# Kernel optimization log

Hardware: AMD Instinct MI355X
Metric: run time of the kernel (lower is better)

## Reference

```python
import jax, jax.numpy as jnp
import numpy as np

EPS = 1e-12  # torch F.normalize eps


def setup_inputs() -> dict:
    key = jax.random.key(0)
    k1, k2 = jax.random.split(key)
    B, C, H, W = 8, 512, 96, 144
    M, D = 512, 512
    query_source = jax.random.normal(k1, (B, C, H, W), dtype=jnp.float32)
    mem = jax.random.uniform(k2, (M, D), dtype=jnp.float32)
    # Memory params are initialized as F.normalize(rand, dim=1)
    mem = mem / jnp.maximum(jnp.linalg.norm(mem, axis=1, keepdims=True), EPS)
    return {"query_source": query_source, "memory": mem}


def reference(query_source, memory):
    # forward(query_source, keys, only_update=False, query_target=None, fusion_keys=None)
    # -> self.read(normalize(query_source).permute(0,2,3,1), memory['3_0'])
    # L2-normalize over channel dim (dim=1), like F.normalize
    norm = jnp.linalg.norm(query_source, axis=1, keepdims=True)
    q = query_source / jnp.maximum(norm, EPS)
    q = jnp.transpose(q, (0, 2, 3, 1))  # [B, H, W, D]
    B, H, W, D = q.shape
    M = memory.shape[0]
    # get_score: score = query @ mem^T, then softmax over tokens (dim 0) and slots (dim 1)
    score = jnp.einsum('nd,md->nm', q.reshape(B * H * W, D), memory)  # [N, M]
    softmax_score_query = jax.nn.softmax(score, axis=0)
    softmax_score_memory = jax.nn.softmax(score, axis=1)
    # read: updated_query = score_memory.detach() @ memory
    updated_query = jax.lax.stop_gradient(softmax_score_memory) @ memory  # [N, D]
    updated_query = updated_query.reshape(B, H, W, D).transpose(0, 3, 1, 2)  # [B, D, H, W]
    return updated_query, softmax_score_query, softmax_score_memory
```

## Files before the change

### kernel.cpp

```cpp
#include <hip/hip_runtime.h>
#include <hip/hip_bf16.h>
#include <cstdint>
#include <cstddef>

#define HWIMG 13824
#define NTOK  110592
#define CDIM  512

typedef float  floatx4  __attribute__((ext_vector_type(4)));
typedef __bf16 bf16x8   __attribute__((ext_vector_type(8)));
typedef unsigned short ushortx8 __attribute__((ext_vector_type(8)));

__device__ __forceinline__ unsigned short f2bf(float f) {
  unsigned int u = __float_as_uint(f);
  u += 0x7FFFu + ((u >> 16) & 1u);
  return (unsigned short)(u >> 16);
}
__device__ __forceinline__ float bf2f(unsigned short u) {
  return __uint_as_float(((unsigned int)u) << 16);
}

#define GLL16(g, l)                                                                \
  __builtin_amdgcn_global_load_lds((const __attribute__((address_space(1))) void*)(g), \
                                   (__attribute__((address_space(3))) void*)(l), 16, 0, 0)

__global__ __launch_bounds__(256) void convert_mem_kernel(
    const float* __restrict__ mem, unsigned short* __restrict__ membf,
    unsigned short* __restrict__ memTbf) {
  int g = blockIdx.x * 256 + threadIdx.x;
  int m = g >> 9, d = g & 511;
  unsigned short b = f2bf(mem[g]);
  membf[g] = b;
  memTbf[d * 512 + m] = b;
}

__global__ __launch_bounds__(256) void normalize_kernel(
    const float* __restrict__ qs, unsigned short* __restrict__ qbf) {
  __shared__ float red[4][64];
  __shared__ float inv[64];
  __shared__ float tile[64][65];
  const int t = threadIdx.x;
  const int n0 = blockIdx.x * 64;
  const int b = n0 / HWIMG;
  const int r0 = n0 % HWIMG;
  const float* base = qs + (size_t)b * 512 * HWIMG + r0;
  const int tok = t & 63, cp = t >> 6;

  float ssq = 0.f;
  for (int c = cp; c < 512; c += 4) {
    float x = base[(size_t)c * HWIMG + tok];
    ssq += x * x;
  }
  red[cp][tok] = ssq;
  __syncthreads();
  if (t < 64) {
    float s = red[0][t] + red[1][t] + red[2][t] + red[3][t];
    inv[t] = 1.0f / fmaxf(sqrtf(s), 1e-12f);
  }
  __syncthreads();

  for (int cc = 0; cc < 8; cc++) {
#pragma unroll
    for (int i = 0; i < 16; i++) {
      int cl = (t >> 6) + i * 4;
      tile[cl][tok] = base[(size_t)(cc * 64 + cl) * HWIMG + tok];
    }
    __syncthreads();
    const int c_out = t & 63;
    const int tg = t >> 6;
#pragma unroll
    for (int i = 0; i < 16; i++) {
      int tk = tg * 16 + i;
      float v = tile[c_out][tk] * inv[tk];
      qbf[(size_t)(n0 + tk) * 512 + cc * 64 + c_out] = f2bf(v);
    }
    __syncthreads();
  }
}

#define GEMM_STAGE8(gAp, gBp, kb)                                          \
  GLL16((gAp) + (kb), lA);                                                 \
  GLL16((gAp) + (kb) + 32768, lA + 4096);                                  \
  GLL16((gAp) + (kb) + 65536, lA + 8192);                                  \
  GLL16((gAp) + (kb) + 98304, lA + 12288);                                 \
  GLL16((gBp) + (kb), lB);                                                 \
  GLL16((gBp) + (kb) + 32768, lB + 4096);                                  \
  GLL16((gBp) + (kb) + 65536, lB + 8192);                                  \
  GLL16((gBp) + (kb) + 98304, lB + 12288);

#define GEMM_K_LOOP(gAp, gBp)                                              \
  for (int kb = 0; kb < 1024; kb += 128) {                                 \
    GEMM_STAGE8(gAp, gBp, kb)                                              \
    asm volatile("s_waitcnt vmcnt(0)" ::: "memory");                       \
    __syncthreads();                                                       \
    _Pragma("unroll")                                                      \
    for (int h = 0; h < 2; h++) {                                          \
      bf16x8 af[4], bfv[4];                                                \
      _Pragma("unroll")                                                    \
      for (int i = 0; i < 4; i++)                                          \
        af[i] = *(const bf16x8*)&Alds[((((am + i) * 2 + h) << 6) | lane) * 8]; \
      _Pragma("unroll")                                                    \
      for (int j = 0; j < 4; j++)                                          \
        bfv[j] = *(const bf16x8*)&Blds[((((bn + j) * 2 + h) << 6) | lane) * 8]; \
      _Pragma("unroll")                                                    \
      for (int i = 0; i < 4; i++)                                          \
        _Pragma("unroll")                                                  \
        for (int j = 0; j < 4; j++)                                        \
          acc[i][j] = __builtin_amdgcn_mfma_f32_16x16x32_bf16(             \
              af[i], bfv[j], acc[i][j], 0, 0, 0);                          \
    }                                                                      \
    __syncthreads();                                                       \
  }

#define GEMM_COMMON_DECLS                                                  \
  __shared__ unsigned short Alds[128 * 64];                                \
  __shared__ unsigned short Blds[128 * 64];                                \
  const int t = threadIdx.x;                                               \
  const int lane = t & 63, wid = t >> 6;                                   \
  const int quad = lane >> 4, li = lane & 15;                              \
  const int n0 = blockIdx.x * 128;                                         \
  const int am = (wid & 1) * 4, bn = (wid >> 1) * 4;                       \
  const int wm = (wid & 1) * 64, wn = (wid >> 1) * 64;                     \
  const int row0 = ((t >> 7) << 4) | (t & 15);                             \
  const int koff = ((t >> 6) & 1) * 64 + ((t >> 4) & 3) * 16;              \
  char* lA = (char*)Alds + t * 16;                                         \
  char* lB = (char*)Blds + t * 16;

__global__ __launch_bounds__(256) void gemm1_kernel(
    const unsigned short* __restrict__ A, const unsigned short* __restrict__ Bm,
    unsigned short* __restrict__ Ebf, float* __restrict__ colsum,
    float* __restrict__ rowsum) {
  __shared__ float cs_lds[512];
  __shared__ float rs_lds[128];
  GEMM_COMMON_DECLS
  cs_lds[t] = 0.f; cs_lds[t + 256] = 0.f;
  if (t < 128) rs_lds[t] = 0.f;
  const char* gA = (const char*)A + (size_t)(n0 + row0) * 1024 + koff;
  const char* gB0 = (const char*)Bm + (size_t)row0 * 1024 + koff;
  float racc[4][4];
#pragma unroll
  for (int i = 0; i < 4; i++)
#pragma unroll
    for (int r = 0; r < 4; r++) racc[i][r] = 0.f;

#pragma unroll 1
  for (int mt = 0; mt < 4; mt++) {
    floatx4 acc[4][4];
    {
      floatx4 z = {0.f, 0.f, 0.f, 0.f};
#pragma unroll
      for (int i = 0; i < 4; i++)
#pragma unroll
        for (int j = 0; j < 4; j++) acc[i][j] = z;
    }
    const char* gB = gB0 + (size_t)mt * 131072;
    GEMM_K_LOOP(gA, gB)

    float cp[4] = {0.f, 0.f, 0.f, 0.f};
#pragma unroll
    for (int i = 0; i < 4; i++) {
#pragma unroll
      for (int r = 0; r < 4; r++) {
        const int row = n0 + wm + i * 16 + quad * 4 + r;
        float rowacc = 0.f;
#pragma unroll
        for (int j = 0; j < 4; j++) {
          float e = __expf(acc[i][j][r]);
          const int col = mt * 128 + wn + j * 16 + li;
          Ebf[(size_t)row * 512 + col] = f2bf(e);
          cp[j] += e;
          rowacc += e;
        }
        racc[i][r] += rowacc;
      }
    }
#pragma unroll
    for (int j = 0; j < 4; j++) {
      float c = cp[j];
      c += __shfl_xor(c, 16, 64);
      c += __shfl_xor(c, 32, 64);
      if (lane < 16) atomicAdd(&cs_lds[mt * 128 + wn + j * 16 + li], c);
    }
  }

#pragma unroll
  for (int i = 0; i < 4; i++) {
#pragma unroll
    for (int r = 0; r < 4; r++) {
      float v = racc[i][r];
      v += __shfl_xor(v, 1, 64);
      v += __shfl_xor(v, 2, 64);
      v += __shfl_xor(v, 4, 64);
      v += __shfl_xor(v, 8, 64);
      if (li == 0) atomicAdd(&rs_lds[wm + i * 16 + quad * 4 + r], v);
    }
  }
  __syncthreads();
  if (t < 128) rowsum[n0 + t] = rs_lds[t];
  atomicAdd(&colsum[t], cs_lds[t]);
  atomicAdd(&colsum[t + 256], cs_lds[t + 256]);
}

__global__ __launch_bounds__(256) void gemm2_kernel(
    const unsigned short* __restrict__ P, const unsigned short* __restrict__ BmT,
    const float* __restrict__ rowsum, float* __restrict__ out0) {
  GEMM_COMMON_DECLS
  const char* gA = (const char*)P + (size_t)(n0 + row0) * 1024 + koff;
  const char* gB0 = (const char*)BmT + (size_t)row0 * 1024 + koff;
  floatx4 rinv[4];
#pragma unroll
  for (int i = 0; i < 4; i++) {
    floatx4 one = {1.f, 1.f, 1.f, 1.f};
    rinv[i] = one / *(const floatx4*)&rowsum[n0 + wm + i * 16 + quad * 4];
  }
  const int bimg = n0 / HWIMG;
  const int r0 = n0 % HWIMG;

#pragma unroll 1
  for (int mt = 0; mt < 4; mt++) {
    floatx4 acc[4][4];
    {
      floatx4 z = {0.f, 0.f, 0.f, 0.f};
#pragma unroll
      for (int i = 0; i < 4; i++)
#pragma unroll
        for (int j = 0; j < 4; j++) acc[i][j] = z;
    }
    const char* gB = gB0 + (size_t)mt * 131072;
    GEMM_K_LOOP(gA, gB)

#pragma unroll
    for (int i = 0; i < 4; i++) {
      const int rb = r0 + wm + i * 16 + quad * 4;
#pragma unroll
      for (int j = 0; j < 4; j++) {
        const int col = mt * 128 + wn + j * 16 + li;
        *(floatx4*)&out0[(size_t)(bimg * 512 + col) * HWIMG + rb] =
            acc[i][j] * rinv[i];
      }
    }
  }
}

__global__ __launch_bounds__(256) void finalize_kernel(
    const unsigned short* __restrict__ Ebf, const float* __restrict__ colsum,
    const float* __restrict__ rowsum, float* __restrict__ out1,
    float* __restrict__ out2) {
  const int t = threadIdx.x;
  const int lane = t & 63, wid = t >> 6;
  const int rowbase = (blockIdx.x * 4 + wid) * 16;
  const int c0 = lane * 8;
  floatx4 one = {1.f, 1.f, 1.f, 1.f};
  floatx4 rc0 = one / *(const floatx4*)&colsum[c0];
  floatx4 rc1 = one / *(const floatx4*)&colsum[c0 + 4];
#pragma unroll 4
  for (int it = 0; it < 16; it++) {
    const int row = rowbase + it;
    const size_t off = (size_t)row * 512 + c0;
    ushortx8 ev = *(const ushortx8*)&Ebf[off];
    floatx4 e0, e1;
    e0[0] = bf2f(ev[0]); e0[1] = bf2f(ev[1]); e0[2] = bf2f(ev[2]); e0[3] = bf2f(ev[3]);
    e1[0] = bf2f(ev[4]); e1[1] = bf2f(ev[5]); e1[2] = bf2f(ev[6]); e1[3] = bf2f(ev[7]);
    float rr = 1.0f / rowsum[row];
    *(floatx4*)&out1[off]     = e0 * rc0;
    *(floatx4*)&out1[off + 4] = e1 * rc1;
    *(floatx4*)&out2[off]     = e0 * rr;
    *(floatx4*)&out2[off + 4] = e1 * rr;
  }
}

extern "C" void kernel_launch(void* const* d_in, const int* in_sizes, int n_in,
                              void* d_out, int out_size, void* d_ws, size_t ws_size,
                              hipStream_t stream) {
  const float* qs  = (const float*)d_in[0];
  const float* mem = (const float*)d_in[1];

  float* out0 = (float*)d_out;
  float* out1 = out0 + (size_t)NTOK * 512;
  float* out2 = out1 + (size_t)NTOK * 512;

  char* ws = (char*)d_ws;
  unsigned short* qbf    = (unsigned short*)ws;
  unsigned short* Ebf    = (unsigned short*)(ws + 113246208);
  unsigned short* membf  = (unsigned short*)(ws + 226492416);
  unsigned short* memTbf = (unsigned short*)(ws + 227016704);
  float* colsum          = (float*)(ws + 227540992);
  float* rowsum          = (float*)(ws + 227543040);

  hipMemsetAsync(colsum, 0, 2048, stream);
  convert_mem_kernel<<<1024, 256, 0, stream>>>(mem, membf, memTbf);
  normalize_kernel<<<NTOK / 64, 256, 0, stream>>>(qs, qbf);
  gemm1_kernel<<<NTOK / 128, 256, 0, stream>>>(qbf, membf, Ebf, colsum, rowsum);
  finalize_kernel<<<NTOK / 64, 256, 0, stream>>>(Ebf, colsum, rowsum, out1, out2);
  gemm2_kernel<<<NTOK / 128, 256, 0, stream>>>(Ebf, memTbf, rowsum, out0);
}
```

Measured before the change: 1.229 ms.

## Double-buffer GEMM K-loop and fuse finalize into gemm2 via staged LDS tiles

Both GEMMs now stream their K and M tiles as one flat loop of 32 stages, using a two-buffer LDS pipeline so global-to-LDS loads of the next stage overlap the MFMA work on the current one. The separate finalize kernel is removed. gemm2 now builds both softmax outputs from the E tiles it already has in LDS during its first 8 stages, scaling by the inverse column and row sums. This avoids re-reading the bf16 E matrix from HBM and one kernel launch. In exchange LDS use doubles to 64KB per block, and gemm2 gets more output store traffic inside the GEMM loop.

```diff
diff --git a/kernel.cpp b/kernel.cpp
--- a/kernel.cpp
+++ b/kernel.cpp
@@ -78,43 +78,8 @@
   }
 }
 
-#define GEMM_STAGE8(gAp, gBp, kb)                                          \
-  GLL16((gAp) + (kb), lA);                                                 \
-  GLL16((gAp) + (kb) + 32768, lA + 4096);                                  \
-  GLL16((gAp) + (kb) + 65536, lA + 8192);                                  \
-  GLL16((gAp) + (kb) + 98304, lA + 12288);                                 \
-  GLL16((gBp) + (kb), lB);                                                 \
-  GLL16((gBp) + (kb) + 32768, lB + 4096);                                  \
-  GLL16((gBp) + (kb) + 65536, lB + 8192);                                  \
-  GLL16((gBp) + (kb) + 98304, lB + 12288);
-
-#define GEMM_K_LOOP(gAp, gBp)                                              \
-  for (int kb = 0; kb < 1024; kb += 128) {                                 \
-    GEMM_STAGE8(gAp, gBp, kb)                                              \
-    asm volatile("s_waitcnt vmcnt(0)" ::: "memory");                       \
-    __syncthreads();                                                       \
-    _Pragma("unroll")                                                      \
-    for (int h = 0; h < 2; h++) {                                          \
-      bf16x8 af[4], bfv[4];                                                \
-      _Pragma("unroll")                                                    \
-      for (int i = 0; i < 4; i++)                                          \
-        af[i] = *(const bf16x8*)&Alds[((((am + i) * 2 + h) << 6) | lane) * 8]; \
-      _Pragma("unroll")                                                    \
-      for (int j = 0; j < 4; j++)                                          \
-        bfv[j] = *(const bf16x8*)&Blds[((((bn + j) * 2 + h) << 6) | lane) * 8]; \
-      _Pragma("unroll")                                                    \
-      for (int i = 0; i < 4; i++)                                          \
-        _Pragma("unroll")                                                  \
-        for (int j = 0; j < 4; j++)                                        \
-          acc[i][j] = __builtin_amdgcn_mfma_f32_16x16x32_bf16(             \
-              af[i], bfv[j], acc[i][j], 0, 0, 0);                          \
-    }                                                                      \
-    __syncthreads();                                                       \
-  }
-
-#define GEMM_COMMON_DECLS                                                  \
-  __shared__ unsigned short Alds[128 * 64];                                \
-  __shared__ unsigned short Blds[128 * 64];                                \
+#define GEMM_DECLS                                                         \
+  __shared__ unsigned short lds[32768];       \
   const int t = threadIdx.x;                                               \
   const int lane = t & 63, wid = t >> 6;                                   \
   const int quad = lane >> 4, li = lane & 15;                              \
@@ -123,16 +88,57 @@
   const int wm = (wid & 1) * 64, wn = (wid >> 1) * 64;                     \
   const int row0 = ((t >> 7) << 4) | (t & 15);                             \
   const int koff = ((t >> 6) & 1) * 64 + ((t >> 4) & 3) * 16;              \
-  char* lA = (char*)Alds + t * 16;                                         \
-  char* lB = (char*)Blds + t * 16;
-
-__global__ __launch_bounds__(256) void gemm1_kernel(
+  char* ldsb = (char*)lds;
+
+#define STAGE(buf, sidx) do {                                              \
+    const char* a_ = gA + (((sidx) & 7) << 7);                             \
+    const char* b_ = gB0 + (((sidx) >> 3) * 131072) + (((sidx) & 7) << 7); \
+    char* la_ = ldsb + (buf) * 32768 + t * 16;                             \
+    char* lb_ = la_ + 16384;                                               \
+    GLL16(a_, la_);          GLL16(a_ + 32768, la_ + 4096);                \
+    GLL16(a_ + 65536, la_ + 8192); GLL16(a_ + 98304, la_ + 12288);         \
+    GLL16(b_, lb_);          GLL16(b_ + 32768, lb_ + 4096);                \
+    GLL16(b_ + 65536, lb_ + 8192); GLL16(b_ + 98304, lb_ + 12288);         \
+  } while (0)
+
+#define COMPUTE(buf) do {                                                  \
+    const unsigned short* Ac = lds + (buf) * 16384;                        \
+    const unsigned short* Bc = Ac + 8192;                                  \
+    _Pragma("unroll")                                                      \
+    for (int h = 0; h < 2; h++) {                                          \
+      bf16x8 af[4], bfv[4];                                                \
+      _Pragma("unroll")                                                    \
+      for (int i = 0; i < 4; i++)                                          \
+        af[i] = *(const bf16x8*)&Ac[((((am + i) * 2 + h) << 6) | lane) * 8]; \
+      _Pragma("unroll")                                                    \
+      for (int j = 0; j < 4; j++)                                          \
+        bfv[j] = *(const bf16x8*)&Bc[((((bn + j) * 2 + h) << 6) | lane) * 8]; \
+      _Pragma("unroll")                                                    \
+      for (int i = 0; i < 4; i++)                                          \
+        _Pragma("unroll")                                                  \
+        for (int j = 0; j < 4; j++)                                        \
+          acc[i][j] = __builtin_amdgcn_mfma_f32_16x16x32_bf16(             \
+              af[i], bfv[j], acc[i][j], 0, 0, 0);                          \
+    }                                                                      \
+  } while (0)
+
+#define ACC_ZERO do {                                                     \
+    floatx4 z_ = {0.f, 0.f, 0.f, 0.f};                                    \
+    _Pragma("unroll")                                                     \
+    for (int i = 0; i < 4; i++)                                           \
+      _Pragma("unroll")                                                   \
+      for (int j = 0; j < 4; j++) acc[i][j] = z_;                         \
+  } while (0)
+
+#define VMCNT0 asm volatile("s_waitcnt vmcnt(0)" ::: "memory")
+
+__global__ __launch_bounds__(256, 2) void gemm1_kernel(
     const unsigned short* __restrict__ A, const unsigned short* __restrict__ Bm,
     unsigned short* __restrict__ Ebf, float* __restrict__ colsum,
     float* __restrict__ rowsum) {
+  GEMM_DECLS
   __shared__ float cs_lds[512];
   __shared__ float rs_lds[128];
-  GEMM_COMMON_DECLS
   cs_lds[t] = 0.f; cs_lds[t + 256] = 0.f;
   if (t < 128) rs_lds[t] = 0.f;
   const char* gA = (const char*)A + (size_t)(n0 + row0) * 1024 + koff;
@@ -142,44 +148,47 @@
   for (int i = 0; i < 4; i++)
 #pragma unroll
     for (int r = 0; r < 4; r++) racc[i][r] = 0.f;
-
+  floatx4 acc[4][4];
+  ACC_ZERO;
+
+  STAGE(0, 0);
+  VMCNT0;
+  __syncthreads();
 #pragma unroll 1
-  for (int mt = 0; mt < 4; mt++) {
-    floatx4 acc[4][4];
-    {
-      floatx4 z = {0.f, 0.f, 0.f, 0.f};
-#pragma unroll
-      for (int i = 0; i < 4; i++)
-#pragma unroll
-        for (int j = 0; j < 4; j++) acc[i][j] = z;
-    }
-    const char* gB = gB0 + (size_t)mt * 131072;
-    GEMM_K_LOOP(gA, gB)
-
-    float cp[4] = {0.f, 0.f, 0.f, 0.f};
-#pragma unroll
-    for (int i = 0; i < 4; i++) {
-#pragma unroll
-      for (int r = 0; r < 4; r++) {
-        const int row = n0 + wm + i * 16 + quad * 4 + r;
-        float rowacc = 0.f;
-#pragma unroll
-        for (int j = 0; j < 4; j++) {
-          float e = __expf(acc[i][j][r]);
-          const int col = mt * 128 + wn + j * 16 + li;
-          Ebf[(size_t)row * 512 + col] = f2bf(e);
-          cp[j] += e;
-          rowacc += e;
+  for (int s = 0; s < 32; ++s) {
+    const int cur = s & 1;
+    if (s < 31) STAGE(cur ^ 1, s + 1);
+    COMPUTE(cur);
+    VMCNT0;
+    __syncthreads();
+    if ((s & 7) == 7) {
+      const int mt = s >> 3;
+      float cp[4] = {0.f, 0.f, 0.f, 0.f};
+#pragma unroll
+      for (int i = 0; i < 4; i++) {
+#pragma unroll
+        for (int r = 0; r < 4; r++) {
+          const int row = n0 + wm + i * 16 + quad * 4 + r;
+          float rowacc = 0.f;
+#pragma unroll
+          for (int j = 0; j < 4; j++) {
+            float e = __expf(acc[i][j][r]);
+            const int col = mt * 128 + wn + j * 16 + li;
+            Ebf[(size_t)row * 512 + col] = f2bf(e);
+            cp[j] += e;
+            rowacc += e;
+          }
+          racc[i][r] += rowacc;
         }
-        racc[i][r] += rowacc;
       }
-    }
-#pragma unroll
-    for (int j = 0; j < 4; j++) {
-      float c = cp[j];
-      c += __shfl_xor(c, 16, 64);
-      c += __shfl_xor(c, 32, 64);
-      if (lane < 16) atomicAdd(&cs_lds[mt * 128 + wn + j * 16 + li], c);
+#pragma unroll
+      for (int j = 0; j < 4; j++) {
+        float c = cp[j];
+        c += __shfl_xor(c, 16, 64);
+        c += __shfl_xor(c, 32, 64);
+        if (lane < 16) atomicAdd(&cs_lds[mt * 128 + wn + j * 16 + li], c);
+      }
+      ACC_ZERO;
     }
   }
 
@@ -201,71 +210,66 @@
   atomicAdd(&colsum[t + 256], cs_lds[t + 256]);
 }
 
-__global__ __launch_bounds__(256) void gemm2_kernel(
+__global__ __launch_bounds__(256, 2) void gemm2_kernel(
     const unsigned short* __restrict__ P, const unsigned short* __restrict__ BmT,
-    const float* __restrict__ rowsum, float* __restrict__ out0) {
-  GEMM_COMMON_DECLS
+    const float* __restrict__ rowsum, const float* __restrict__ colsum,
+    float* __restrict__ out0, float* __restrict__ out1, float* __restrict__ out2) {
+  GEMM_DECLS
+  __shared__ __align__(16) float inv_cs[512];
+  __shared__ __align__(16) float inv_rs[128];
+  inv_cs[t] = 1.0f / colsum[t];
+  inv_cs[t + 256] = 1.0f / colsum[t + 256];
+  if (t < 128) inv_rs[t] = 1.0f / rowsum[n0 + t];
   const char* gA = (const char*)P + (size_t)(n0 + row0) * 1024 + koff;
   const char* gB0 = (const char*)BmT + (size_t)row0 * 1024 + koff;
-  floatx4 rinv[4];
-#pragma unroll
-  for (int i = 0; i < 4; i++) {
-    floatx4 one = {1.f, 1.f, 1.f, 1.f};
-    rinv[i] = one / *(const floatx4*)&rowsum[n0 + wm + i * 16 + quad * 4];
-  }
   const int bimg = n0 / HWIMG;
   const int r0 = n0 % HWIMG;
-
+  floatx4 acc[4][4];
+  ACC_ZERO;
+
+  STAGE(0, 0);
+  VMCNT0;
+  __syncthreads();
 #pragma unroll 1
-  for (int mt = 0; mt < 4; mt++) {
-    floatx4 acc[4][4];
-    {
-      floatx4 z = {0.f, 0.f, 0.f, 0.f};
-#pragma unroll
-      for (int i = 0; i < 4; i++)
-#pragma unroll
-        for (int j = 0; j < 4; j++) acc[i][j] = z;
-    }
-    const char* gB = gB0 + (size_t)mt * 131072;
-    GEMM_K_LOOP(gA, gB)
-
-#pragma unroll
-    for (int i = 0; i < 4; i++) {
-      const int rb = r0 + wm + i * 16 + quad * 4;
-#pragma unroll
-      for (int j = 0; j < 4; j++) {
-        const int col = mt * 128 + wn + j * 16 + li;
-        *(floatx4*)&out0[(size_t)(bimg * 512 + col) * HWIMG + rb] =
-            acc[i][j] * rinv[i];
+  for (int s = 0; s < 32; ++s) {
+    const int cur = s & 1;
+    if (s < 31) STAGE(cur ^ 1, s + 1);
+    COMPUTE(cur);
+    VMCNT0;
+    __syncthreads();
+    if (s < 8) {
+      const int cbase = s * 64 + (koff >> 1);
+      const floatx4 rca = *(const floatx4*)&inv_cs[cbase];
+      const floatx4 rcb = *(const floatx4*)&inv_cs[cbase + 4];
+#pragma unroll
+      for (int sh = 0; sh < 4; ++sh) {
+        ushortx8 ev = *(const ushortx8*)(ldsb + cur * 32768 + t * 16 + sh * 4096);
+        const float rr = inv_rs[row0 + 32 * sh];
+        floatx4 e0, e1;
+        e0[0] = bf2f(ev[0]); e0[1] = bf2f(ev[1]); e0[2] = bf2f(ev[2]); e0[3] = bf2f(ev[3]);
+        e1[0] = bf2f(ev[4]); e1[1] = bf2f(ev[5]); e1[2] = bf2f(ev[6]); e1[3] = bf2f(ev[7]);
+        const size_t off = (size_t)(n0 + row0 + 32 * sh) * 512 + cbase;
+        *(floatx4*)&out1[off]     = e0 * rca;
+        *(floatx4*)&out1[off + 4] = e1 * rcb;
+        *(floatx4*)&out2[off]     = e0 * rr;
+        *(floatx4*)&out2[off + 4] = e1 * rr;
       }
     }
-  }
-}
-
-__global__ __launch_bounds__(256) void finalize_kernel(
-    const unsigned short* __restrict__ Ebf, const float* __restrict__ colsum,
-    const float* __restrict__ rowsum, float* __restrict__ out1,
-    float* __restrict__ out2) {
-  const int t = threadIdx.x;
-  const int lane = t & 63, wid = t >> 6;
-  const int rowbase = (blockIdx.x * 4 + wid) * 16;
-  const int c0 = lane * 8;
-  floatx4 one = {1.f, 1.f, 1.f, 1.f};
-  floatx4 rc0 = one / *(const floatx4*)&colsum[c0];
-  floatx4 rc1 = one / *(const floatx4*)&colsum[c0 + 4];
-#pragma unroll 4
-  for (int it = 0; it < 16; it++) {
-    const int row = rowbase + it;
-    const size_t off = (size_t)row * 512 + c0;
-    ushortx8 ev = *(const ushortx8*)&Ebf[off];
-    floatx4 e0, e1;
-    e0[0] = bf2f(ev[0]); e0[1] = bf2f(ev[1]); e0[2] = bf2f(ev[2]); e0[3] = bf2f(ev[3]);
-    e1[0] = bf2f(ev[4]); e1[1] = bf2f(ev[5]); e1[2] = bf2f(ev[6]); e1[3] = bf2f(ev[7]);
-    float rr = 1.0f / rowsum[row];
-    *(floatx4*)&out1[off]     = e0 * rc0;
-    *(floatx4*)&out1[off + 4] = e1 * rc1;
-    *(floatx4*)&out2[off]     = e0 * rr;
-    *(floatx4*)&out2[off + 4] = e1 * rr;
+    if ((s & 7) == 7) {
+      const int mt = s >> 3;
+#pragma unroll
+      for (int i = 0; i < 4; i++) {
+        const int rb = r0 + wm + i * 16 + quad * 4;
+        const floatx4 riv = *(const floatx4*)&inv_rs[wm + i * 16 + quad * 4];
+#pragma unroll
+        for (int j = 0; j < 4; j++) {
+          const int col = mt * 128 + wn + j * 16 + li;
+          *(floatx4*)&out0[(size_t)(bimg * 512 + col) * HWIMG + rb] =
+              acc[i][j] * riv;
+        }
+      }
+      ACC_ZERO;
+    }
   }
 }
 
@@ -291,6 +295,6 @@
   convert_mem_kernel<<<1024, 256, 0, stream>>>(mem, membf, memTbf);
   normalize_kernel<<<NTOK / 64, 256, 0, stream>>>(qs, qbf);
   gemm1_kernel<<<NTOK / 128, 256, 0, stream>>>(qbf, membf, Ebf, colsum, rowsum);
-  finalize_kernel<<<NTOK / 64, 256, 0, stream>>>(Ebf, colsum, rowsum, out1, out2);
-  gemm2_kernel<<<NTOK / 128, 256, 0, stream>>>(Ebf, memTbf, rowsum, out0);
-}
+  gemm2_kernel<<<NTOK / 128, 256, 0, stream>>>(Ebf, memTbf, rowsum, colsum,
+                                               out0, out1, out2);
+}
```

Result: no change. 1.211 ms (-1.5%).
